# Kernel optimization log

Hardware: AMD Instinct MI355X
Metric: run time of the kernel (lower is better)

The kernel has to match this reference:

```python
import jax, jax.numpy as jnp
import numpy as np

N_NODES = 50000
N_EDGES = 500000
IN_CH = 128
OUT_CH = 256


def setup_inputs() -> dict:
    key = jax.random.key(0)
    k1, k2, k3, k4, k5 = jax.random.split(key, 5)
    x = jax.random.normal(k1, (N_NODES, IN_CH), dtype=jnp.float32)
    edge_index = jax.random.randint(k2, (2, N_EDGES), 0, N_NODES, dtype=jnp.int64)
    edge_weight = jax.random.normal(k3, (N_EDGES,), dtype=jnp.float32)
    # GCNConv linear weight (xavier-uniform) and bias (zeros in torch init; use randn for generality)
    limit = float(np.sqrt(6.0 / (IN_CH + OUT_CH)))
    W = jax.random.uniform(k4, (IN_CH, OUT_CH), minval=-limit, maxval=limit, dtype=jnp.float32)
    b = jnp.zeros((OUT_CH,), dtype=jnp.float32)
    return {"x": x, "W": W, "b": b, "edge_index": edge_index, "edge_weight": edge_weight}


def reference(x, W, b, edge_index, edge_weight):
    N = x.shape[0]
    # GCN wrapper applies sigmoid to edge weights before GCNConv
    ew = jax.nn.sigmoid(edge_weight)
    # gcn_norm: add self-loops with weight 1
    loop = jnp.arange(N, dtype=edge_index.dtype)
    row = jnp.concatenate([edge_index[0], loop])  # source nodes
    col = jnp.concatenate([edge_index[1], loop])  # target nodes
    w = jnp.concatenate([ew, jnp.ones((N,), dtype=x.dtype)])
    # degree on target index, symmetric normalization
    deg = jax.ops.segment_sum(w, col, num_segments=N)
    dinv = jnp.where(deg > 0, jax.lax.rsqrt(deg), jnp.zeros_like(deg))
    norm = dinv[row] * w * dinv[col]  # [E+N]
    # linear transform first (GCNConv: lin has no bias; bias added after aggregation)
    h = x @ W  # [N, OUT_CH]
    msg = h[row] * norm[:, None]  # gather + scale  [E+N, OUT_CH]
    out = jax.ops.segment_sum(msg, col, num_segments=N) + b
    return out
```

## Files before the change

kernel.cpp:

```cpp
#include <hip/hip_runtime.h>
#include <hip/hip_bf16.h>
#include <hip/hip_fp16.h>
#include <math.h>

#define NN 50000
#define NE 500000
#define IC 128
#define OC 256
#define NPAD 50176
#define NB 196
#define NEB 1954
#define CAP 64

typedef short bf16x8 __attribute__((ext_vector_type(8)));
typedef float f32x4 __attribute__((ext_vector_type(4)));

static __device__ inline unsigned short f2b(float f) {
    __hip_bfloat16 h = __float2bfloat16(f);
    return *reinterpret_cast<unsigned short*>(&h);
}
static __device__ inline float b2f(short u) {
    unsigned v = ((unsigned)(unsigned short)u) << 16;
    return __int_as_float(v);
}
static __device__ inline float h2f(unsigned short h) {
    __half v = __ushort_as_half(h);
    return __half2float(v);
}

__global__ void k_init(unsigned long long* __restrict__ deg64) {
    int i = blockIdx.x * 256 + threadIdx.x;
    deg64[i] = (unsigned long long)(1u << 24);
}

__global__ void k_pass1(const int* __restrict__ row,
                        const int* __restrict__ col,
                        const float* __restrict__ ew,
                        unsigned long long* __restrict__ deg64,
                        unsigned* __restrict__ epack,
                        const float* __restrict__ W,
                        unsigned short* __restrict__ WT) {
    int g = blockIdx.x * 256 + threadIdx.x;
    if (g < NE) {
        int c = col[g];
        float w = 1.0f / (1.0f + expf(-ew[g]));
        unsigned long long pack = (1ull << 32) | (unsigned long long)(unsigned)(w * 16777216.0f);
        unsigned long long old = atomicAdd(&deg64[c], pack);
        int ord = (int)(old >> 32);
        if (ord < CAP) {
            unsigned short wh = __half_as_ushort(__float2half_rn(w));
            unsigned p = ((unsigned)wh << 16) | (unsigned)row[g];
            epack[(size_t)c * CAP + ord] = p;
        }
    }
    if (g < IC * OC) {
        int k = g >> 8;
        int n = g & 255;
        WT[n * IC + k] = f2b(W[g]);
    }
}

__global__ __launch_bounds__(256) void k_scale(
        const unsigned long long* __restrict__ deg64,
        const float* __restrict__ x,
        unsigned short* __restrict__ xb,
        float* __restrict__ dinv) {
    int t = threadIdx.x;
    int n = blockIdx.x * 16 + (t >> 4);
    int l = t & 15;
    unsigned long long v = deg64[n];
    float deg = (float)(unsigned)v * (1.0f / 16777216.0f);
    float di = rsqrtf(deg);
    if (l == 0) dinv[n] = di;
    const float4* xr = (const float4*)(x + (size_t)n * IC + l * 8);
    float4 a0 = xr[0], a1 = xr[1];
    bf16x8 o;
    o[0] = (short)f2b(a0.x * di); o[1] = (short)f2b(a0.y * di);
    o[2] = (short)f2b(a0.z * di); o[3] = (short)f2b(a0.w * di);
    o[4] = (short)f2b(a1.x * di); o[5] = (short)f2b(a1.y * di);
    o[6] = (short)f2b(a1.z * di); o[7] = (short)f2b(a1.w * di);
    ((bf16x8*)xb)[(size_t)n * 16 + l] = o;
}

__global__ __launch_bounds__(256) void k_gather_gemm(
        const unsigned short* __restrict__ xb,
        const unsigned long long* __restrict__ deg64,
        const unsigned* __restrict__ epack,
        const float* __restrict__ dinv,
        const unsigned short* __restrict__ WT,
        const float* __restrict__ bias,
        float* __restrict__ out) {
    __shared__ __align__(16) unsigned short a[32][136];

    const int base = blockIdx.x * 32;
    const int g = threadIdx.x >> 3;
    const int l8 = threadIdx.x & 7;
    const int n = base + g;
    const bf16x8* xv = (const bf16x8*)xb;

    float acc[16];
    if (n < NN) {
        float di = dinv[n];
        unsigned long long dv = deg64[n];
        int cnt = (int)(dv >> 32);
        if (cnt > CAP) cnt = CAP;

        bf16x8 xs0 = xv[(size_t)n * 16 + l8];
        bf16x8 xs1 = xv[(size_t)n * 16 + 8 + l8];
        #pragma unroll
        for (int c = 0; c < 8; ++c) { acc[c] = b2f(xs0[c]) * di; acc[8 + c] = b2f(xs1[c]) * di; }

        const unsigned* ep = epack + (size_t)n * CAP;
        uint4 q = *(const uint4*)ep;
        int e = 0;
        for (; e + 4 <= cnt; e += 4) {
            uint4 cur = q;
            q = *(const uint4*)(ep + e + 4);
            int r0 = (int)(cur.x & 0xFFFFu);
            int r1 = (int)(cur.y & 0xFFFFu);
            int r2 = (int)(cur.z & 0xFFFFu);
            int r3 = (int)(cur.w & 0xFFFFu);
            float w0 = h2f((unsigned short)(cur.x >> 16)) * di;
            float w1 = h2f((unsigned short)(cur.y >> 16)) * di;
            float w2 = h2f((unsigned short)(cur.z >> 16)) * di;
            float w3 = h2f((unsigned short)(cur.w >> 16)) * di;
            bf16x8 v00 = xv[(size_t)r0 * 16 + l8];
            bf16x8 v01 = xv[(size_t)r0 * 16 + 8 + l8];
            bf16x8 v10 = xv[(size_t)r1 * 16 + l8];
            bf16x8 v11 = xv[(size_t)r1 * 16 + 8 + l8];
            bf16x8 v20 = xv[(size_t)r2 * 16 + l8];
            bf16x8 v21 = xv[(size_t)r2 * 16 + 8 + l8];
            bf16x8 v30 = xv[(size_t)r3 * 16 + l8];
            bf16x8 v31 = xv[(size_t)r3 * 16 + 8 + l8];
            #pragma unroll
            for (int c = 0; c < 8; ++c) { acc[c] += b2f(v00[c]) * w0; acc[8 + c] += b2f(v01[c]) * w0; }
            #pragma unroll
            for (int c = 0; c < 8; ++c) { acc[c] += b2f(v10[c]) * w1; acc[8 + c] += b2f(v11[c]) * w1; }
            #pragma unroll
            for (int c = 0; c < 8; ++c) { acc[c] += b2f(v20[c]) * w2; acc[8 + c] += b2f(v21[c]) * w2; }
            #pragma unroll
            for (int c = 0; c < 8; ++c) { acc[c] += b2f(v30[c]) * w3; acc[8 + c] += b2f(v31[c]) * w3; }
        }
        for (; e < cnt; ++e) {
            unsigned p = ep[e];
            int r = (int)(p & 0xFFFFu);
            float w = h2f((unsigned short)(p >> 16)) * di;
            bf16x8 v0 = xv[(size_t)r * 16 + l8];
            bf16x8 v1 = xv[(size_t)r * 16 + 8 + l8];
            #pragma unroll
            for (int c = 0; c < 8; ++c) { acc[c] += b2f(v0[c]) * w; acc[8 + c] += b2f(v1[c]) * w; }
        }
    } else {
        #pragma unroll
        for (int c = 0; c < 16; ++c) acc[c] = 0.0f;
    }

    bf16x8 o0, o1;
    #pragma unroll
    for (int c = 0; c < 8; ++c) { o0[c] = (short)f2b(acc[c]); o1[c] = (short)f2b(acc[8 + c]); }
    *(bf16x8*)(&a[g][l8 * 8]) = o0;
    *(bf16x8*)(&a[g][64 + l8 * 8]) = o1;

    __syncthreads();

    const int w = threadIdx.x >> 6;
    const int lane = threadIdx.x & 63;
    const int n0 = w * 64;
    const int lm = lane & 15;
    const int lk = (lane >> 4) * 8;

    f32x4 acc4[2][4] = {};
    #pragma unroll
    for (int ks = 0; ks < 4; ++ks) {
        const int k0 = ks * 32 + lk;
        bf16x8 wf[4], af[2];
        #pragma unroll
        for (int j = 0; j < 4; ++j)
            wf[j] = *(const bf16x8*)(WT + (size_t)(n0 + j * 16 + lm) * IC + k0);
        #pragma unroll
        for (int i = 0; i < 2; ++i)
            af[i] = *(const bf16x8*)(&a[i * 16 + lm][k0]);
        #pragma unroll
        for (int i = 0; i < 2; ++i)
            #pragma unroll
            for (int j = 0; j < 4; ++j)
                acc4[i][j] = __builtin_amdgcn_mfma_f32_16x16x32_bf16(wf[j], af[i], acc4[i][j], 0, 0, 0);
    }

    const int mcol = lane & 15;
    const int nb4 = (lane >> 4) * 4;
    #pragma unroll
    for (int i = 0; i < 2; ++i) {
        int m = base + i * 16 + mcol;
        if (m < NN) {
            #pragma unroll
            for (int j = 0; j < 4; ++j) {
                int nn = n0 + j * 16 + nb4;
                float4 bv = *(const float4*)&bias[nn];
                float4 ov;
                ov.x = acc4[i][j][0] + bv.x;
                ov.y = acc4[i][j][1] + bv.y;
                ov.z = acc4[i][j][2] + bv.z;
                ov.w = acc4[i][j][3] + bv.w;
                *(float4*)(out + (size_t)m * OC + nn) = ov;
            }
        }
    }
}

extern "C" void kernel_launch(void* const* d_in, const int* in_sizes, int n_in,
                              void* d_out, int out_size, void* d_ws, size_t ws_size,
                              hipStream_t stream) {
    const float* x  = (const float*)d_in[0];
    const float* W  = (const float*)d_in[1];
    const float* b  = (const float*)d_in[2];
    const int*   ei = (const int*)d_in[3];
    const float* ew = (const float*)d_in[4];
    const int* row = ei;
    const int* col = ei + NE;
    float* out = (float*)d_out;

    char* w0 = (char*)d_ws;
    unsigned long long* deg64 = (unsigned long long*)w0;  w0 += NPAD * 8;
    float* dinv  = (float*)w0;                   w0 += NPAD * 4;
    unsigned* epack = (unsigned*)w0;             w0 += ((size_t)NPAD * CAP + 128) * 4;
    unsigned short* WT   = (unsigned short*)w0;  w0 += IC * OC * 2;
    unsigned short* xb   = (unsigned short*)w0;

    k_init       <<<NB, 256, 0, stream>>>(deg64);
    k_pass1      <<<NEB, 256, 0, stream>>>(row, col, ew, deg64, epack, W, WT);
    k_scale      <<<NN / 16, 256, 0, stream>>>(deg64, x, xb, dinv);
    k_gather_gemm<<<(NN + 31) / 32, 256, 0, stream>>>(xb, deg64, epack, dinv, WT, b, out);
}
```

Baseline: 162.2 us.

## Bucket incoming edges by source-row range and gather with fixed unrolled batches

Incoming edges per target node are now split into four buckets by source-node range (r>>14), each with its own counter and capacity of 24, and the degree counter becomes a separate 32-bit atomic. The gather kernel loads the first four slots of every bucket and issues eight predicated row loads at once, with overflow loops for the rest. This aims to raise memory-level parallelism and improve source-row locality in the gather. In exchange it adds a second atomic per edge, a larger edge buffer, and wasted loads to row 0 for empty slots.

```diff
diff --git a/kernel.cpp b/kernel.cpp
--- a/kernel.cpp
+++ b/kernel.cpp
@@ -10,7 +10,9 @@
 #define NPAD 50176
 #define NB 196
 #define NEB 1954
-#define CAP 64
+#define NBKT 4
+#define CAPB 24
+#define SLOTS (NBKT * CAPB)
 
 typedef short bf16x8 __attribute__((ext_vector_type(8)));
 typedef float f32x4 __attribute__((ext_vector_type(4)));
@@ -28,29 +30,33 @@
     return __half2float(v);
 }
 
-__global__ void k_init(unsigned long long* __restrict__ deg64) {
+__global__ void k_init(unsigned* __restrict__ deg,
+                       uint4* __restrict__ bcnt) {
     int i = blockIdx.x * 256 + threadIdx.x;
-    deg64[i] = (unsigned long long)(1u << 24);
+    deg[i] = 1u << 24;
+    bcnt[i] = make_uint4(0, 0, 0, 0);
 }
 
 __global__ void k_pass1(const int* __restrict__ row,
                         const int* __restrict__ col,
                         const float* __restrict__ ew,
-                        unsigned long long* __restrict__ deg64,
+                        unsigned* __restrict__ deg,
+                        unsigned* __restrict__ bcnt,
                         unsigned* __restrict__ epack,
                         const float* __restrict__ W,
                         unsigned short* __restrict__ WT) {
     int g = blockIdx.x * 256 + threadIdx.x;
     if (g < NE) {
         int c = col[g];
+        int r = row[g];
         float w = 1.0f / (1.0f + expf(-ew[g]));
-        unsigned long long pack = (1ull << 32) | (unsigned long long)(unsigned)(w * 16777216.0f);
-        unsigned long long old = atomicAdd(&deg64[c], pack);
-        int ord = (int)(old >> 32);
-        if (ord < CAP) {
+        atomicAdd(&deg[c], (unsigned)(w * 16777216.0f));
+        int b = r >> 14;
+        unsigned ord = atomicAdd(&bcnt[c * NBKT + b], 1u);
+        if (ord < CAPB) {
             unsigned short wh = __half_as_ushort(__float2half_rn(w));
-            unsigned p = ((unsigned)wh << 16) | (unsigned)row[g];
-            epack[(size_t)c * CAP + ord] = p;
+            unsigned p = ((unsigned)wh << 16) | (unsigned)r;
+            epack[(size_t)c * SLOTS + b * CAPB + ord] = p;
         }
     }
     if (g < IC * OC) {
@@ -61,16 +67,15 @@
 }
 
 __global__ __launch_bounds__(256) void k_scale(
-        const unsigned long long* __restrict__ deg64,
+        const unsigned* __restrict__ deg,
         const float* __restrict__ x,
         unsigned short* __restrict__ xb,
         float* __restrict__ dinv) {
     int t = threadIdx.x;
     int n = blockIdx.x * 16 + (t >> 4);
     int l = t & 15;
-    unsigned long long v = deg64[n];
-    float deg = (float)(unsigned)v * (1.0f / 16777216.0f);
-    float di = rsqrtf(deg);
+    float dg = (float)deg[n] * (1.0f / 16777216.0f);
+    float di = rsqrtf(dg);
     if (l == 0) dinv[n] = di;
     const float4* xr = (const float4*)(x + (size_t)n * IC + l * 8);
     float4 a0 = xr[0], a1 = xr[1];
@@ -82,9 +87,30 @@
     ((bf16x8*)xb)[(size_t)n * 16 + l] = o;
 }
 
+#define MEDGE(word, cc, jj, rr, ww)                                          \
+    int rr = ((cc) > (jj)) ? (int)((word) & 0xFFFFu) : 0;                    \
+    float ww = ((cc) > (jj)) ? h2f((unsigned short)((word) >> 16)) * di : 0.0f;
+
+#define LROW(rr, v0, v1)                                                     \
+    bf16x8 v0 = xv[(size_t)(rr) * 16 + l8];                                  \
+    bf16x8 v1 = xv[(size_t)(rr) * 16 + 8 + l8];
+
+#define FMAR(v0, v1, ww)                                                     \
+    _Pragma("unroll")                                                        \
+    for (int c = 0; c < 8; ++c) { acc[c] += b2f(v0[c]) * (ww); acc[8 + c] += b2f(v1[c]) * (ww); }
+
+#define OFLOW(bp, cc)                                                        \
+    for (int e = 4; e < (cc); ++e) {                                         \
+        unsigned p = (bp)[e];                                                \
+        int r_ = (int)(p & 0xFFFFu);                                         \
+        float w_ = h2f((unsigned short)(p >> 16)) * di;                      \
+        LROW(r_, q0_, q1_)                                                   \
+        FMAR(q0_, q1_, w_)                                                   \
+    }
+
 __global__ __launch_bounds__(256) void k_gather_gemm(
         const unsigned short* __restrict__ xb,
-        const unsigned long long* __restrict__ deg64,
+        const unsigned* __restrict__ bcnt,
         const unsigned* __restrict__ epack,
         const float* __restrict__ dinv,
         const unsigned short* __restrict__ WT,
@@ -101,54 +127,53 @@
     float acc[16];
     if (n < NN) {
         float di = dinv[n];
-        unsigned long long dv = deg64[n];
-        int cnt = (int)(dv >> 32);
-        if (cnt > CAP) cnt = CAP;
+        uint4 bc = *(const uint4*)(bcnt + (size_t)n * NBKT);
+        int c0 = bc.x < CAPB ? (int)bc.x : CAPB;
+        int c1 = bc.y < CAPB ? (int)bc.y : CAPB;
+        int c2 = bc.z < CAPB ? (int)bc.z : CAPB;
+        int c3 = bc.w < CAPB ? (int)bc.w : CAPB;
+        const unsigned* ep = epack + (size_t)n * SLOTS;
+        uint4 h0 = *(const uint4*)(ep);
+        uint4 h1 = *(const uint4*)(ep + CAPB);
+        uint4 h2 = *(const uint4*)(ep + 2 * CAPB);
+        uint4 h3 = *(const uint4*)(ep + 3 * CAPB);
 
         bf16x8 xs0 = xv[(size_t)n * 16 + l8];
         bf16x8 xs1 = xv[(size_t)n * 16 + 8 + l8];
         #pragma unroll
         for (int c = 0; c < 8; ++c) { acc[c] = b2f(xs0[c]) * di; acc[8 + c] = b2f(xs1[c]) * di; }
 
-        const unsigned* ep = epack + (size_t)n * CAP;
-        uint4 q = *(const uint4*)ep;
-        int e = 0;
-        for (; e + 4 <= cnt; e += 4) {
-            uint4 cur = q;
-            q = *(const uint4*)(ep + e + 4);
-            int r0 = (int)(cur.x & 0xFFFFu);
-            int r1 = (int)(cur.y & 0xFFFFu);
-            int r2 = (int)(cur.z & 0xFFFFu);
-            int r3 = (int)(cur.w & 0xFFFFu);
-            float w0 = h2f((unsigned short)(cur.x >> 16)) * di;
-            float w1 = h2f((unsigned short)(cur.y >> 16)) * di;
-            float w2 = h2f((unsigned short)(cur.z >> 16)) * di;
-            float w3 = h2f((unsigned short)(cur.w >> 16)) * di;
-            bf16x8 v00 = xv[(size_t)r0 * 16 + l8];
-            bf16x8 v01 = xv[(size_t)r0 * 16 + 8 + l8];
-            bf16x8 v10 = xv[(size_t)r1 * 16 + l8];
-            bf16x8 v11 = xv[(size_t)r1 * 16 + 8 + l8];
-            bf16x8 v20 = xv[(size_t)r2 * 16 + l8];
-            bf16x8 v21 = xv[(size_t)r2 * 16 + 8 + l8];
-            bf16x8 v30 = xv[(size_t)r3 * 16 + l8];
-            bf16x8 v31 = xv[(size_t)r3 * 16 + 8 + l8];
-            #pragma unroll
-            for (int c = 0; c < 8; ++c) { acc[c] += b2f(v00[c]) * w0; acc[8 + c] += b2f(v01[c]) * w0; }
-            #pragma unroll
-            for (int c = 0; c < 8; ++c) { acc[c] += b2f(v10[c]) * w1; acc[8 + c] += b2f(v11[c]) * w1; }
-            #pragma unroll
-            for (int c = 0; c < 8; ++c) { acc[c] += b2f(v20[c]) * w2; acc[8 + c] += b2f(v21[c]) * w2; }
-            #pragma unroll
-            for (int c = 0; c < 8; ++c) { acc[c] += b2f(v30[c]) * w3; acc[8 + c] += b2f(v31[c]) * w3; }
-        }
-        for (; e < cnt; ++e) {
-            unsigned p = ep[e];
-            int r = (int)(p & 0xFFFFu);
-            float w = h2f((unsigned short)(p >> 16)) * di;
-            bf16x8 v0 = xv[(size_t)r * 16 + l8];
-            bf16x8 v1 = xv[(size_t)r * 16 + 8 + l8];
-            #pragma unroll
-            for (int c = 0; c < 8; ++c) { acc[c] += b2f(v0[c]) * w; acc[8 + c] += b2f(v1[c]) * w; }
+        {
+            MEDGE(h0.x, c0, 0, rA, wA)  MEDGE(h0.y, c0, 1, rB, wB)
+            MEDGE(h0.z, c0, 2, rC, wC)  MEDGE(h0.w, c0, 3, rD, wD)
+            MEDGE(h1.x, c1, 0, rE, wE)  MEDGE(h1.y, c1, 1, rF, wF)
+            MEDGE(h1.z, c1, 2, rG, wG)  MEDGE(h1.w, c1, 3, rH, wH)
+            LROW(rA, vA0, vA1)  LROW(rB, vB0, vB1)
+            LROW(rC, vC0, vC1)  LROW(rD, vD0, vD1)
+            LROW(rE, vE0, vE1)  LROW(rF, vF0, vF1)
+            LROW(rG, vG0, vG1)  LROW(rH, vH0, vH1)
+            FMAR(vA0, vA1, wA)  FMAR(vB0, vB1, wB)
+            FMAR(vC0, vC1, wC)  FMAR(vD0, vD1, wD)
+            FMAR(vE0, vE1, wE)  FMAR(vF0, vF1, wF)
+            FMAR(vG0, vG1, wG)  FMAR(vH0, vH1, wH)
+            if (c0 > 4) { OFLOW(ep, c0) }
+            if (c1 > 4) { OFLOW(ep + CAPB, c1) }
+        }
+        {
+            MEDGE(h2.x, c2, 0, rA, wA)  MEDGE(h2.y, c2, 1, rB, wB)
+            MEDGE(h2.z, c2, 2, rC, wC)  MEDGE(h2.w, c2, 3, rD, wD)
+            MEDGE(h3.x, c3, 0, rE, wE)  MEDGE(h3.y, c3, 1, rF, wF)
+            MEDGE(h3.z, c3, 2, rG, wG)  MEDGE(h3.w, c3, 3, rH, wH)
+            LROW(rA, vA0, vA1)  LROW(rB, vB0, vB1)
+            LROW(rC, vC0, vC1)  LROW(rD, vD0, vD1)
+            LROW(rE, vE0, vE1)  LROW(rF, vF0, vF1)
+            LROW(rG, vG0, vG1)  LROW(rH, vH0, vH1)
+            FMAR(vA0, vA1, wA)  FMAR(vB0, vB1, wB)
+            FMAR(vC0, vC1, wC)  FMAR(vD0, vD1, wD)
+            FMAR(vE0, vE1, wE)  FMAR(vF0, vF1, wF)
+            FMAR(vG0, vG1, wG)  FMAR(vH0, vH1, wH)
+            if (c2 > 4) { OFLOW(ep + 2 * CAPB, c2) }
+            if (c3 > 4) { OFLOW(ep + 3 * CAPB, c3) }
         }
     } else {
         #pragma unroll
@@ -221,14 +246,15 @@
     float* out = (float*)d_out;
 
     char* w0 = (char*)d_ws;
-    unsigned long long* deg64 = (unsigned long long*)w0;  w0 += NPAD * 8;
+    unsigned* deg  = (unsigned*)w0;              w0 += NPAD * 4;
     float* dinv  = (float*)w0;                   w0 += NPAD * 4;
-    unsigned* epack = (unsigned*)w0;             w0 += ((size_t)NPAD * CAP + 128) * 4;
+    unsigned* bcnt = (unsigned*)w0;              w0 += (size_t)NPAD * NBKT * 4;
+    unsigned* epack = (unsigned*)w0;             w0 += ((size_t)NPAD * SLOTS + 128) * 4;
     unsigned short* WT   = (unsigned short*)w0;  w0 += IC * OC * 2;
     unsigned short* xb   = (unsigned short*)w0;
 
-    k_init       <<<NB, 256, 0, stream>>>(deg64);
-    k_pass1      <<<NEB, 256, 0, stream>>>(row, col, ew, deg64, epack, W, WT);
-    k_scale      <<<NN / 16, 256, 0, stream>>>(deg64, x, xb, dinv);
-    k_gather_gemm<<<(NN + 31) / 32, 256, 0, stream>>>(xb, deg64, epack, dinv, WT, b, out);
-}
+    k_init       <<<NB, 256, 0, stream>>>(deg, (uint4*)bcnt);
+    k_pass1      <<<NEB, 256, 0, stream>>>(row, col, ew, deg, bcnt, epack, W, WT);
+    k_scale      <<<NN / 16, 256, 0, stream>>>(deg, x, xb, dinv);
+    k_gather_gemm<<<(NN + 31) / 32, 256, 0, stream>>>(xb, bcnt, epack, dinv, WT, b, out);
+}
```

New measurement: 188.1 us. 1.16x slower.

## Split feature gather into four column slices and separate GEMM kernel

Applied to the files above, without the earlier changes.

Stores scaled bf16 features in four 32-column slices and runs the neighbor gather once per slice. Each pass then touches a 3.2 MB table that is more likely to stay in cache, instead of the full 12.8 MB table. The aggregated result is written to a sliced buffer in global memory and a separate MFMA GEMM kernel reads it. This costs an extra global round trip for the aggregate, reads the edge lists four times, and adds kernel launches.

```diff
diff --git a/kernel.cpp b/kernel.cpp
--- a/kernel.cpp
+++ b/kernel.cpp
@@ -11,8 +11,11 @@
 #define NB 196
 #define NEB 1954
 #define CAP 64
+#define NSL 4
+#define SLICEU ((size_t)NPAD * 32)
 
 typedef short bf16x8 __attribute__((ext_vector_type(8)));
+typedef short bf16x4 __attribute__((ext_vector_type(4)));
 typedef float f32x4 __attribute__((ext_vector_type(4)));
 
 static __device__ inline unsigned short f2b(float f) {
@@ -63,7 +66,7 @@
 __global__ __launch_bounds__(256) void k_scale(
         const unsigned long long* __restrict__ deg64,
         const float* __restrict__ x,
-        unsigned short* __restrict__ xb,
+        unsigned short* __restrict__ xbs,
         float* __restrict__ dinv) {
     int t = threadIdx.x;
     int n = blockIdx.x * 16 + (t >> 4);
@@ -79,130 +82,119 @@
     o[2] = (short)f2b(a0.z * di); o[3] = (short)f2b(a0.w * di);
     o[4] = (short)f2b(a1.x * di); o[5] = (short)f2b(a1.y * di);
     o[6] = (short)f2b(a1.z * di); o[7] = (short)f2b(a1.w * di);
-    ((bf16x8*)xb)[(size_t)n * 16 + l] = o;
-}
-
-__global__ __launch_bounds__(256) void k_gather_gemm(
-        const unsigned short* __restrict__ xb,
+    *(bf16x8*)(xbs + (size_t)(l >> 2) * SLICEU + (size_t)n * 32 + (l & 3) * 8) = o;
+}
+
+__global__ __launch_bounds__(256) void k_gather(
+        const unsigned short* __restrict__ xbs,
         const unsigned long long* __restrict__ deg64,
         const unsigned* __restrict__ epack,
         const float* __restrict__ dinv,
-        const unsigned short* __restrict__ WT,
-        const float* __restrict__ bias,
-        float* __restrict__ out) {
-    __shared__ __align__(16) unsigned short a[32][136];
-
+        unsigned short* __restrict__ aggs,
+        int s) {
     const int base = blockIdx.x * 32;
     const int g = threadIdx.x >> 3;
     const int l8 = threadIdx.x & 7;
     const int n = base + g;
-    const bf16x8* xv = (const bf16x8*)xb;
-
-    float acc[16];
-    if (n < NN) {
-        float di = dinv[n];
-        unsigned long long dv = deg64[n];
-        int cnt = (int)(dv >> 32);
-        if (cnt > CAP) cnt = CAP;
-
-        bf16x8 xs0 = xv[(size_t)n * 16 + l8];
-        bf16x8 xs1 = xv[(size_t)n * 16 + 8 + l8];
-        #pragma unroll
-        for (int c = 0; c < 8; ++c) { acc[c] = b2f(xs0[c]) * di; acc[8 + c] = b2f(xs1[c]) * di; }
-
-        const unsigned* ep = epack + (size_t)n * CAP;
-        uint4 q = *(const uint4*)ep;
-        int e = 0;
-        for (; e + 4 <= cnt; e += 4) {
-            uint4 cur = q;
-            q = *(const uint4*)(ep + e + 4);
-            int r0 = (int)(cur.x & 0xFFFFu);
-            int r1 = (int)(cur.y & 0xFFFFu);
-            int r2 = (int)(cur.z & 0xFFFFu);
-            int r3 = (int)(cur.w & 0xFFFFu);
-            float w0 = h2f((unsigned short)(cur.x >> 16)) * di;
-            float w1 = h2f((unsigned short)(cur.y >> 16)) * di;
-            float w2 = h2f((unsigned short)(cur.z >> 16)) * di;
-            float w3 = h2f((unsigned short)(cur.w >> 16)) * di;
-            bf16x8 v00 = xv[(size_t)r0 * 16 + l8];
-            bf16x8 v01 = xv[(size_t)r0 * 16 + 8 + l8];
-            bf16x8 v10 = xv[(size_t)r1 * 16 + l8];
-            bf16x8 v11 = xv[(size_t)r1 * 16 + 8 + l8];
-            bf16x8 v20 = xv[(size_t)r2 * 16 + l8];
-            bf16x8 v21 = xv[(size_t)r2 * 16 + 8 + l8];
-            bf16x8 v30 = xv[(size_t)r3 * 16 + l8];
-            bf16x8 v31 = xv[(size_t)r3 * 16 + 8 + l8];
-            #pragma unroll
-            for (int c = 0; c < 8; ++c) { acc[c] += b2f(v00[c]) * w0; acc[8 + c] += b2f(v01[c]) * w0; }
-            #pragma unroll
-            for (int c = 0; c < 8; ++c) { acc[c] += b2f(v10[c]) * w1; acc[8 + c] += b2f(v11[c]) * w1; }
-            #pragma unroll
-            for (int c = 0; c < 8; ++c) { acc[c] += b2f(v20[c]) * w2; acc[8 + c] += b2f(v21[c]) * w2; }
-            #pragma unroll
-            for (int c = 0; c < 8; ++c) { acc[c] += b2f(v30[c]) * w3; acc[8 + c] += b2f(v31[c]) * w3; }
-        }
-        for (; e < cnt; ++e) {
-            unsigned p = ep[e];
-            int r = (int)(p & 0xFFFFu);
-            float w = h2f((unsigned short)(p >> 16)) * di;
-            bf16x8 v0 = xv[(size_t)r * 16 + l8];
-            bf16x8 v1 = xv[(size_t)r * 16 + 8 + l8];
-            #pragma unroll
-            for (int c = 0; c < 8; ++c) { acc[c] += b2f(v0[c]) * w; acc[8 + c] += b2f(v1[c]) * w; }
-        }
-    } else {
-        #pragma unroll
-        for (int c = 0; c < 16; ++c) acc[c] = 0.0f;
-    }
-
-    bf16x8 o0, o1;
-    #pragma unroll
-    for (int c = 0; c < 8; ++c) { o0[c] = (short)f2b(acc[c]); o1[c] = (short)f2b(acc[8 + c]); }
-    *(bf16x8*)(&a[g][l8 * 8]) = o0;
-    *(bf16x8*)(&a[g][64 + l8 * 8]) = o1;
-
-    __syncthreads();
-
+    if (n >= NN) return;
+
+    const unsigned short* xsl = xbs + (size_t)s * SLICEU;
+    float di = dinv[n];
+    unsigned long long dv = deg64[n];
+    int cnt = (int)(dv >> 32);
+    if (cnt > CAP) cnt = CAP;
+
+    bf16x4 xs = *(const bf16x4*)(xsl + (size_t)n * 32 + l8 * 4);
+    float acc[4];
+    #pragma unroll
+    for (int c = 0; c < 4; ++c) acc[c] = b2f(xs[c]) * di;
+
+    const unsigned* ep = epack + (size_t)n * CAP;
+    uint4 q = *(const uint4*)ep;
+    int e = 0;
+    for (; e + 4 <= cnt; e += 4) {
+        uint4 cur = q;
+        q = *(const uint4*)(ep + e + 4);
+        int r0 = (int)(cur.x & 0xFFFFu);
+        int r1 = (int)(cur.y & 0xFFFFu);
+        int r2 = (int)(cur.z & 0xFFFFu);
+        int r3 = (int)(cur.w & 0xFFFFu);
+        float w0 = h2f((unsigned short)(cur.x >> 16)) * di;
+        float w1 = h2f((unsigned short)(cur.y >> 16)) * di;
+        float w2 = h2f((unsigned short)(cur.z >> 16)) * di;
+        float w3 = h2f((unsigned short)(cur.w >> 16)) * di;
+        bf16x4 v0 = *(const bf16x4*)(xsl + (size_t)r0 * 32 + l8 * 4);
+        bf16x4 v1 = *(const bf16x4*)(xsl + (size_t)r1 * 32 + l8 * 4);
+        bf16x4 v2 = *(const bf16x4*)(xsl + (size_t)r2 * 32 + l8 * 4);
+        bf16x4 v3 = *(const bf16x4*)(xsl + (size_t)r3 * 32 + l8 * 4);
+        #pragma unroll
+        for (int c = 0; c < 4; ++c) acc[c] += b2f(v0[c]) * w0;
+        #pragma unroll
+        for (int c = 0; c < 4; ++c) acc[c] += b2f(v1[c]) * w1;
+        #pragma unroll
+        for (int c = 0; c < 4; ++c) acc[c] += b2f(v2[c]) * w2;
+        #pragma unroll
+        for (int c = 0; c < 4; ++c) acc[c] += b2f(v3[c]) * w3;
+    }
+    for (; e < cnt; ++e) {
+        unsigned p = ep[e];
+        int r = (int)(p & 0xFFFFu);
+        float w = h2f((unsigned short)(p >> 16)) * di;
+        bf16x4 v = *(const bf16x4*)(xsl + (size_t)r * 32 + l8 * 4);
+        #pragma unroll
+        for (int c = 0; c < 4; ++c) acc[c] += b2f(v[c]) * w;
+    }
+
+    bf16x4 o;
+    #pragma unroll
+    for (int c = 0; c < 4; ++c) o[c] = (short)f2b(acc[c]);
+    *(bf16x4*)(aggs + (size_t)s * SLICEU + (size_t)n * 32 + l8 * 4) = o;
+}
+
+__global__ __launch_bounds__(256) void k_gemm(const unsigned short* __restrict__ aggs,
+                                              const unsigned short* __restrict__ WT,
+                                              const float* __restrict__ bias,
+                                              float* __restrict__ out) {
     const int w = threadIdx.x >> 6;
     const int lane = threadIdx.x & 63;
-    const int n0 = w * 64;
+    const int m0 = blockIdx.y * 64 + (w >> 1) * 32;
+    const int n0 = blockIdx.x * 128 + (w & 1) * 64;
     const int lm = lane & 15;
     const int lk = (lane >> 4) * 8;
 
-    f32x4 acc4[2][4] = {};
+    f32x4 acc[2][4] = {};
     #pragma unroll
     for (int ks = 0; ks < 4; ++ks) {
-        const int k0 = ks * 32 + lk;
         bf16x8 wf[4], af[2];
         #pragma unroll
         for (int j = 0; j < 4; ++j)
-            wf[j] = *(const bf16x8*)(WT + (size_t)(n0 + j * 16 + lm) * IC + k0);
+            wf[j] = *(const bf16x8*)(WT + (size_t)(n0 + j * 16 + lm) * IC + ks * 32 + lk);
         #pragma unroll
         for (int i = 0; i < 2; ++i)
-            af[i] = *(const bf16x8*)(&a[i * 16 + lm][k0]);
+            af[i] = *(const bf16x8*)(aggs + (size_t)ks * SLICEU + (size_t)(m0 + i * 16 + lm) * 32 + lk);
         #pragma unroll
         for (int i = 0; i < 2; ++i)
             #pragma unroll
             for (int j = 0; j < 4; ++j)
-                acc4[i][j] = __builtin_amdgcn_mfma_f32_16x16x32_bf16(wf[j], af[i], acc4[i][j], 0, 0, 0);
+                acc[i][j] = __builtin_amdgcn_mfma_f32_16x16x32_bf16(wf[j], af[i], acc[i][j], 0, 0, 0);
     }
 
     const int mcol = lane & 15;
     const int nb4 = (lane >> 4) * 4;
     #pragma unroll
     for (int i = 0; i < 2; ++i) {
-        int m = base + i * 16 + mcol;
+        int m = m0 + i * 16 + mcol;
         if (m < NN) {
             #pragma unroll
             for (int j = 0; j < 4; ++j) {
                 int nn = n0 + j * 16 + nb4;
                 float4 bv = *(const float4*)&bias[nn];
-                float4 ov;
-                ov.x = acc4[i][j][0] + bv.x;
-                ov.y = acc4[i][j][1] + bv.y;
-                ov.z = acc4[i][j][2] + bv.z;
-                ov.w = acc4[i][j][3] + bv.w;
-                *(float4*)(out + (size_t)m * OC + nn) = ov;
+                float4 o;
+                o.x = acc[i][j][0] + bv.x;
+                o.y = acc[i][j][1] + bv.y;
+                o.z = acc[i][j][2] + bv.z;
+                o.w = acc[i][j][3] + bv.w;
+                *(float4*)(out + (size_t)m * OC + nn) = o;
             }
         }
     }
@@ -225,10 +217,13 @@
     float* dinv  = (float*)w0;                   w0 += NPAD * 4;
     unsigned* epack = (unsigned*)w0;             w0 += ((size_t)NPAD * CAP + 128) * 4;
     unsigned short* WT   = (unsigned short*)w0;  w0 += IC * OC * 2;
-    unsigned short* xb   = (unsigned short*)w0;
-
-    k_init       <<<NB, 256, 0, stream>>>(deg64);
-    k_pass1      <<<NEB, 256, 0, stream>>>(row, col, ew, deg64, epack, W, WT);
-    k_scale      <<<NN / 16, 256, 0, stream>>>(deg64, x, xb, dinv);
-    k_gather_gemm<<<(NN + 31) / 32, 256, 0, stream>>>(xb, deg64, epack, dinv, WT, b, out);
-}
+    unsigned short* xbs  = (unsigned short*)w0;  w0 += NSL * SLICEU * 2;
+    unsigned short* aggs = (unsigned short*)w0;
+
+    k_init  <<<NB, 256, 0, stream>>>(deg64);
+    k_pass1 <<<NEB, 256, 0, stream>>>(row, col, ew, deg64, epack, W, WT);
+    k_scale <<<NN / 16, 256, 0, stream>>>(deg64, x, xbs, dinv);
+    for (int s = 0; s < NSL; ++s)
+        k_gather<<<(NN + 31) / 32, 256, 0, stream>>>(xbs, deg64, epack, dinv, aggs, s);
+    k_gemm  <<<dim3(2, (NN + 63) / 64), 256, 0, stream>>>(aggs, WT, b, out);
+}
```

After: 181.8 us. 12.0% more time.
